# Optimization experiments

Hardware: AMD Instinct MI355X
Metric: run time of the kernel (lower is better)

## Reference

```python
import jax, jax.numpy as jnp
import numpy as np

# Model dims
C = 16          # in_channels / d_model
D_INNER = 64    # expand * C, expand = 64 // C = 4
HEADDIM = 4
NHEADS = D_INNER // HEADDIM   # 16
D_STATE = 64
D_CONV = 4
CONV_DIM = D_INNER + 2 * D_STATE        # 192 (x, B, C streams)
D_IN_PROJ = 2 * D_INNER + 2 * D_STATE + NHEADS  # 272 (z, xBC, dt)
# Input volume
BSZ, DD, HH, WW = 8, 32, 16, 16
L = DD * HH * WW  # 8192, multiple of 256 -> exact adaptive max pool
POOL = 256


def setup_inputs():
    key = jax.random.key(0)
    ks = jax.random.split(key, 10)
    x = jax.random.normal(ks[0], (BSZ, C, DD, HH, WW), jnp.float32)
    # 3 independent Mamba2 blocks -> stack params with leading dim 3
    Win = jax.random.normal(ks[1], (3, D_IN_PROJ, C), jnp.float32) / np.sqrt(C).astype(np.float32)
    conv_w = jax.random.normal(ks[2], (3, CONV_DIM, D_CONV), jnp.float32) / np.sqrt(D_CONV).astype(np.float32)
    conv_b = jax.random.normal(ks[3], (3, CONV_DIM), jnp.float32) * 0.1
    dt_bias = jax.random.normal(ks[4], (3, NHEADS), jnp.float32) * 0.5
    A_log = jnp.log(jax.random.uniform(ks[5], (3, NHEADS), jnp.float32, minval=1.0, maxval=16.0))
    Dp = jax.random.normal(ks[6], (3, NHEADS), jnp.float32) * 0.5 + 1.0
    norm_w = jnp.ones((3, D_INNER), jnp.float32)
    Wout = jax.random.normal(ks[7], (3, C, D_INNER), jnp.float32) / np.sqrt(D_INNER).astype(np.float32)
    gamma = jnp.ones((3, C), jnp.float32)
    beta = jnp.zeros((3, C), jnp.float32)
    lin_w = jax.random.normal(ks[8], (3, 1, C), jnp.float32) / np.sqrt(C).astype(np.float32)
    lin_b = jnp.zeros((3, 1), jnp.float32)
    return dict(x=x, Win=Win, conv_w=conv_w, conv_b=conv_b, dt_bias=dt_bias,
                A_log=A_log, Dp=Dp, norm_w=norm_w, Wout=Wout,
                gamma=gamma, beta=beta, lin_w=lin_w, lin_b=lin_b)


def _mamba2(u, Win, conv_w, conv_b, dt_bias, A_log, Dp, norm_w, Wout):
    """Mamba2 block: u (B, L, C) -> (B, L, C). ngroups=1, rmsnorm gated."""
    B, Lx, _ = u.shape
    zxbcdt = jnp.einsum('blc,pc->blp', u, Win)  # (B, L, 272)
    z = zxbcdt[..., :D_INNER]
    xBC = zxbcdt[..., D_INNER:D_INNER + CONV_DIM]
    dt = jax.nn.softplus(zxbcdt[..., D_INNER + CONV_DIM:] + dt_bias)  # (B, L, H)
    # causal depthwise conv over time
    conv = jax.lax.conv_general_dilated(
        jnp.transpose(xBC, (0, 2, 1)), conv_w[:, None, :], (1,),
        [(D_CONV - 1, 0)], feature_group_count=CONV_DIM)
    xBC = jax.nn.silu(jnp.transpose(conv, (0, 2, 1)) + conv_b)
    xh = xBC[..., :D_INNER].reshape(B, Lx, NHEADS, HEADDIM)
    Bm = xBC[..., D_INNER:D_INNER + D_STATE]   # (B, L, N)
    Cm = xBC[..., D_INNER + D_STATE:]          # (B, L, N)
    A = -jnp.exp(A_log)                        # (H,)
    dA = jnp.exp(dt * A)                       # (B, L, H)
    dtx = dt[..., None] * xh                   # (B, L, H, P)

    def step(S, inp):
        dA_t, dtx_t, B_t, C_t = inp
        S = S * dA_t[:, :, None, None] + dtx_t[..., None] * B_t[:, None, None, :]
        y_t = jnp.einsum('bhpn,bn->bhp', S, C_t)
        return S, y_t

    S0 = jnp.zeros((B, NHEADS, HEADDIM, D_STATE), u.dtype)
    xs = (jnp.moveaxis(dA, 1, 0), jnp.moveaxis(dtx, 1, 0),
          jnp.moveaxis(Bm, 1, 0), jnp.moveaxis(Cm, 1, 0))
    _, ys = jax.lax.scan(step, S0, xs)                       # (L, B, H, P)
    y = jnp.moveaxis(ys, 0, 1) + Dp[None, None, :, None] * xh
    y = y.reshape(B, Lx, D_INNER) * jax.nn.silu(z)           # gate first
    y = y * jax.lax.rsqrt(jnp.mean(y * y, -1, keepdims=True) + 1e-5) * norm_w
    return jnp.einsum('bld,cd->blc', y, Wout)


def _proj_pool(y, gamma, beta, lw, lb):
    """ReLU -> BatchNorm1d (batch stats) -> Linear(C,1) -> AdaptiveMaxPool1d(256)."""
    B, Lx, _ = y.shape
    v = jax.nn.relu(y.reshape(-1, C))
    mu = jnp.mean(v, 0)
    var = jnp.mean((v - mu) ** 2, 0)
    v = (v - mu) * jax.lax.rsqrt(var + 1e-5) * gamma + beta
    s = (v @ lw.T + lb).reshape(B, Lx)
    return jnp.max(s.reshape(B, POOL, Lx // POOL), -1)  # (B, 256)


def reference(x, Win, conv_w, conv_b, dt_bias, A_log, Dp, norm_w, Wout,
              gamma, beta, lin_w, lin_b):
    B, Cc, Dd, Hh, Ww = x.shape
    Lx = Dd * Hh * Ww
    fD = jnp.transpose(x.reshape(B, Cc, Lx), (0, 2, 1))
    fH = jnp.transpose(jnp.transpose(x, (0, 1, 3, 4, 2)).reshape(B, Cc, Lx), (0, 2, 1))
    fW = jnp.transpose(jnp.transpose(x, (0, 1, 4, 2, 3)).reshape(B, Cc, Lx), (0, 2, 1))
    seqs = jnp.stack([fD, fH, fW], 0)  # (3, B, L, C)
    ys = jax.vmap(_mamba2)(seqs, Win, conv_w, conv_b, dt_bias, A_log, Dp, norm_w, Wout)
    pooled = jax.vmap(_proj_pool)(ys, gamma, beta, lin_w, lin_b)  # (3, B, 256)
    return jnp.concatenate([pooled[0], pooled[1], pooled[2]], -1)[:, None, :]  # (B,1,768)
```

## Files before the change

### kernel.cpp

```cpp
#include <hip/hip_runtime.h>
#include <math.h>

#define CONVD 192
#define NC 128
#define PW 32
#define LOG2E 1.4426950408889634f
#define LN2f  0.69314718055994531f

#define OFF_DST   0u
#define OFF_CHA   4194304u
#define OFF_YS    4210688u
#define OFF_PART  5259264u
#define PD        5292032u

#define XSW(m, t)   ((m) * 64 + (((((t) >> 2) ^ ((m) & 15)) & 15) << 2) + ((t) & 3))
#define XSW4(m, tq) ((m) * 64 + ((((tq) ^ ((m) & 15)) & 15) << 2))

typedef float f32x2 __attribute__((ext_vector_type(2)));

__device__ __forceinline__ f32x2 pk_fma(f32x2 a, f32x2 b, f32x2 c) {
    f32x2 d;
    asm("v_pk_fma_f32 %0, %1, %2, %3" : "=v"(d) : "v"(a), "v"(b), "v"(c));
    return d;
}
__device__ __forceinline__ f32x2 pk_fma_alo(f32x2 a, f32x2 b, f32x2 c) {
    f32x2 d;
    asm("v_pk_fma_f32 %0, %1, %2, %3 op_sel_hi:[0,1,1]" : "=v"(d) : "v"(a), "v"(b), "v"(c));
    return d;
}
__device__ __forceinline__ f32x2 pk_fma_ahi(f32x2 a, f32x2 b, f32x2 c) {
    f32x2 d;
    asm("v_pk_fma_f32 %0, %1, %2, %3 op_sel:[1,0,0]" : "=v"(d) : "v"(a), "v"(b), "v"(c));
    return d;
}
__device__ __forceinline__ f32x2 pk_fma_blo(f32x2 a, f32x2 b, f32x2 c) {
    f32x2 d;
    asm("v_pk_fma_f32 %0, %1, %2, %3 op_sel_hi:[1,0,1]" : "=v"(d) : "v"(a), "v"(b), "v"(c));
    return d;
}
__device__ __forceinline__ f32x2 pk_fma_bhi(f32x2 a, f32x2 b, f32x2 c) {
    f32x2 d;
    asm("v_pk_fma_f32 %0, %1, %2, %3 op_sel:[0,1,0]" : "=v"(d) : "v"(a), "v"(b), "v"(c));
    return d;
}
__device__ __forceinline__ f32x2 lo2(float4 v) { f32x2 r; r.x = v.x; r.y = v.y; return r; }
__device__ __forceinline__ f32x2 hi2(float4 v) { f32x2 r; r.x = v.z; r.y = v.w; return r; }

__device__ __forceinline__ float fast_silu(float x) {
    float e = __builtin_amdgcn_exp2f(-x * LOG2E);
    return x * __builtin_amdgcn_rcpf(1.f + e);
}
__device__ __forceinline__ float fast_softplus(float x) {
    if (x > 20.f) return x;
    float e = __builtin_amdgcn_exp2f(x * LOG2E);
    return LN2f * __builtin_amdgcn_logf(1.f + e);
}

template<int NT>
__device__ __forceinline__ void stage_u(
    const float* __restrict__ x, float* u_s, int b, int l0, int dir, int tid)
{
    for (int i = tid; i < 67 * 16; i += NT) {
        int pos = i >> 4, c = i & 15;
        int l = l0 + pos - 3;
        float v = 0.f;
        if (l >= 0) {
            if (dir == 0) {
                v = x[(b * 16 + c) * 8192 + l];
            } else if (dir == 1) {
                int h = l >> 9, w = (l >> 5) & 15, d = l & 31;
                v = x[(((b * 16 + c) * 32 + d) * 16 + h) * 16 + w];
            } else {
                int w = l >> 9, d = (l >> 4) & 31, h = l & 15;
                v = x[(((b * 16 + c) * 32 + d) * 16 + h) * 16 + w];
            }
        }
        u_s[pos * 17 + c] = v;
    }
}

__device__ __forceinline__ float pk_dot16(const f32x2* u2, const float* wp) {
    float4 w0 = *(const float4*)(wp);
    float4 w1 = *(const float4*)(wp + 4);
    float4 w2 = *(const float4*)(wp + 8);
    float4 w3 = *(const float4*)(wp + 12);
    f32x2 a = {0.f, 0.f};
    a = pk_fma(u2[0], lo2(w0), a);
    a = pk_fma(u2[1], hi2(w0), a);
    a = pk_fma(u2[2], lo2(w1), a);
    a = pk_fma(u2[3], hi2(w1), a);
    a = pk_fma(u2[4], lo2(w2), a);
    a = pk_fma(u2[5], hi2(w2), a);
    a = pk_fma(u2[6], lo2(w3), a);
    a = pk_fma(u2[7], hi2(w3), a);
    return a.x + a.y;
}

__global__ __launch_bounds__(512, 6) void k_delta(
    const float* __restrict__ x, const float* __restrict__ Win,
    const float* __restrict__ convw, const float* __restrict__ convb,
    const float* __restrict__ dtb, const float* __restrict__ A_log,
    float* __restrict__ ws, int dir0, int dslm)
{
    __shared__ float u_s[67 * 17];
    __shared__ float xh_c[4096];
    __shared__ float Bs[4096];
    __shared__ float dts[16 * 65];
    __shared__ float wbuf[16 * 65];
    const int tid = threadIdx.x;
    const int ck = blockIdx.x;
    const int b = blockIdx.y;
    const int dir = dir0 + blockIdx.z;
    float* base = ws + (size_t)(dslm * blockIdx.z) * PD;
    float* Dst = base + OFF_DST;
    float* chA = base + OFF_CHA;
    const int l0 = ck * 64;
    float* halo = wbuf;

    stage_u<512>(x, u_s, b, l0, dir, tid);
    __syncthreads();

    const int lane = tid & 63;
    const int wv = __builtin_amdgcn_readfirstlane(tid >> 6);

    f32x2 u2[8];
    {
        const float* ur = &u_s[(lane + 3) * 17];
        #pragma unroll
        for (int k = 0; k < 8; k++) { u2[k].x = ur[2 * k]; u2[k].y = ur[2 * k + 1]; }
    }
    if (tid < 128) {
        f32x2 uh2[8];
        #pragma unroll
        for (int pos = 0; pos < 3; pos++) {
            const float* uhr = &u_s[pos * 17];
            #pragma unroll
            for (int k = 0; k < 8; k++) { uh2[k].x = uhr[2 * k]; uh2[k].y = uhr[2 * k + 1]; }
            halo[pos * 128 + tid] = pk_dot16(uh2, Win + (size_t)(dir * 272 + 64 + tid) * 16);
        }
    }
    __syncthreads();

    for (int i = 0; i < 18; i++) {
        const int g = wv * 18 + i;
        const int col = (g < 128) ? (64 + g) : (256 + (g - 128));
        float acc = pk_dot16(u2, Win + (size_t)(dir * 272 + col) * 16);
        if (col < 256) {
            const int ch = col - 64;
            float v1 = __shfl_up(acc, 1);
            float v2 = __shfl_up(acc, 2);
            float v3 = __shfl_up(acc, 3);
            float hh0 = halo[ch];
            float hh1 = halo[128 + ch];
            float hh2 = halo[256 + ch];
            float m1 = (lane >= 1) ? v1 : hh2;
            float m2 = (lane >= 2) ? v2 : ((lane == 0) ? hh1 : hh2);
            float m3 = (lane >= 3) ? v3 : ((lane == 0) ? hh0 : ((lane == 1) ? hh1 : hh2));
            const float* cwp = convw + (size_t)(dir * CONVD + ch) * 4;
            float conv = convb[dir * CONVD + ch]
                       + cwp[0] * m3 + cwp[1] * m2 + cwp[2] * m1 + cwp[3] * acc;
            float xv = fast_silu(conv);
            if (ch < 64) xh_c[XSW(ch, lane)] = xv;
            else         Bs[XSW(ch - 64, lane)] = xv;
        } else {
            const int h = col - 256;
            dts[h * 65 + lane] = fast_softplus(acc + dtb[dir * 16 + h]);
        }
    }
    __syncthreads();

    for (int h = wv; h < 16; h += 8) {
        float A2 = -expf(A_log[dir * 16 + h]) * LOG2E;
        float dtv = dts[h * 65 + lane];
        float v = dtv * A2;
        #pragma unroll
        for (int off = 1; off < 64; off <<= 1) {
            float o = __shfl_up(v, off, 64);
            if (lane >= off) v += o;
        }
        float tot = __shfl(v, 63, 64);
        wbuf[h * 65 + lane] = __builtin_amdgcn_exp2f(tot - v) * dtv;
        if (lane == 63) chA[(b * 16 + h) * 128 + ck] = __builtin_amdgcn_exp2f(tot);
    }
    __syncthreads();

    for (int j = tid; j < 4096; j += 512) {
        int hp = j >> 6, t = j & 63;
        xh_c[XSW(hp, t)] *= wbuf[(hp >> 2) * 65 + t];
    }
    __syncthreads();

    if (tid < 256) {
        const int hp4 = tid >> 4, n4 = tid & 15;
        f32x2 a2[4][4] = {};
        for (int tq = 0; tq < 16; tq++) {
            float4 xv[4], bv[4];
            #pragma unroll
            for (int i2 = 0; i2 < 4; i2++) {
                xv[i2] = *(const float4*)&xh_c[XSW4(4 * hp4 + i2, tq)];
                bv[i2] = *(const float4*)&Bs[XSW4(4 * n4 + i2, tq)];
            }
            #pragma unroll
            for (int i2 = 0; i2 < 4; i2++)
                #pragma unroll
                for (int j2 = 0; j2 < 4; j2++) {
                    a2[i2][j2] = pk_fma(lo2(xv[i2]), lo2(bv[j2]), a2[i2][j2]);
                    a2[i2][j2] = pk_fma(hi2(xv[i2]), hi2(bv[j2]), a2[i2][j2]);
                }
        }
        #pragma unroll
        for (int i2 = 0; i2 < 4; i2++) {
            int hp = 4 * hp4 + i2;
            int h = hp >> 2, p = hp & 3;
            *(float4*)(Dst + ((size_t)((b * 16 + h) * 128 + ck)) * 256 + p * 64 + 4 * n4) =
                make_float4(a2[i2][0].x + a2[i2][0].y, a2[i2][1].x + a2[i2][1].y,
                            a2[i2][2].x + a2[i2][2].y, a2[i2][3].x + a2[i2][3].y);
        }
    }
}

__global__ __launch_bounds__(64) void k_chunk_scan(
    float* __restrict__ ws, int dslm)
{
    float* base = ws + (size_t)(dslm * blockIdx.z) * PD;
    float* Dst = base + OFF_DST;
    const float* chA = base + OFF_CHA;
    const int bh = blockIdx.x >> 2;
    const int elem = (blockIdx.x & 3) * 64 + threadIdx.x;
    float S = 0.f;
    for (int k0 = 0; k0 < NC; k0 += 8) {
        float d[8], av[8];
        #pragma unroll
        for (int j = 0; j < 8; j++) {
            d[j] = Dst[((size_t)(bh * 128 + k0 + j)) * 256 + elem];
            av[j] = chA[bh * 128 + k0 + j];
        }
        #pragma unroll
        for (int j = 0; j < 8; j++) {
            Dst[((size_t)(bh * 128 + k0 + j)) * 256 + elem] = S;
            S = av[j] * S + d[j];
        }
    }
}

__global__ __launch_bounds__(512, 4) void k_out_epi(
    const float* __restrict__ x, const float* __restrict__ Win,
    const float* __restrict__ convw, const float* __restrict__ convb,
    const float* __restrict__ dtb, const float* __restrict__ A_log,
    const float* __restrict__ Dp, const float* __restrict__ normw,
    const float* __restrict__ Wout, float* __restrict__ ws, int dir0, int dslm)
{
    __shared__ float SinT[64 * 66];
    __shared__ float xh_c[4096];
    __shared__ float Bz[4096];
    __shared__ float Cy[4352];
    __shared__ float uW[67 * 17];
    __shared__ float dts[16 * 68];
    __shared__ float ct2l[16 * 68];
    __shared__ float Dps[16];
    __shared__ float red[4][34];
    float* base = ws + (size_t)(dslm * blockIdx.z) * PD;
    const float* Dst = base + OFF_DST;
    float* ys        = base + OFF_YS;
    float* partials  = base + OFF_PART;
    const int dir = dir0 + blockIdx.z;
    const int tid = threadIdx.x;
    const int b = blockIdx.y;
    const int ck = blockIdx.x;
    const int l0 = ck * 64;
    const int tg = tid & 255;
    const int t4 = tg >> 4, x4 = tg & 15;
    const int grp = tid >> 8;
    const int lane = tid & 63;
    const int wv = __builtin_amdgcn_readfirstlane(tid >> 6);
    float* halo = ct2l;

    stage_u<512>(x, uW, b, l0, dir, tid);
    for (int j = tid; j < 1024; j += 512) {
        int hp = j >> 4, n4 = (j & 15) << 2;
        int h = hp >> 2, p = hp & 3;
        float4 sv = *(const float4*)(Dst + ((size_t)((b * 16 + h) * 128 + ck)) * 256 + p * 64 + n4);
        SinT[(n4 + 0) * 66 + hp] = sv.x;
        SinT[(n4 + 1) * 66 + hp] = sv.y;
        SinT[(n4 + 2) * 66 + hp] = sv.z;
        SinT[(n4 + 3) * 66 + hp] = sv.w;
    }
    if (tid < 16) Dps[tid] = Dp[dir * 16 + tid];
    __syncthreads();

    f32x2 u2[8];
    {
        const float* ur = &uW[(lane + 3) * 17];
        #pragma unroll
        for (int k = 0; k < 8; k++) { u2[k].x = ur[2 * k]; u2[k].y = ur[2 * k + 1]; }
    }
    if (tid < 192) {
        f32x2 uh2[8];
        #pragma unroll
        for (int pos = 0; pos < 3; pos++) {
            const float* uhr = &uW[pos * 17];
            #pragma unroll
            for (int k = 0; k < 8; k++) { uh2[k].x = uhr[2 * k]; uh2[k].y = uhr[2 * k + 1]; }
            halo[pos * 192 + tid] = pk_dot16(uh2, Win + (size_t)(dir * 272 + 64 + tid) * 16);
        }
    }
    __syncthreads();

    for (int i = 0; i < 26; i++) {
        const int col = 64 + wv * 26 + i;
        float acc = pk_dot16(u2, Win + (size_t)(dir * 272 + col) * 16);
        if (col < 256) {
            const int ch = col - 64;
            float v1 = __shfl_up(acc, 1);
            float v2 = __shfl_up(acc, 2);
            float v3 = __shfl_up(acc, 3);
            float hh0 = halo[ch];
            float hh1 = halo[192 + ch];
            float hh2 = halo[384 + ch];
            float m1 = (lane >= 1) ? v1 : hh2;
            float m2 = (lane >= 2) ? v2 : ((lane == 0) ? hh1 : hh2);
            float m3 = (lane >= 3) ? v3 : ((lane == 0) ? hh0 : ((lane == 1) ? hh1 : hh2));
            const float* cwp = convw + (size_t)(dir * CONVD + ch) * 4;
            float conv = convb[dir * CONVD + ch]
                       + cwp[0] * m3 + cwp[1] * m2 + cwp[2] * m1 + cwp[3] * acc;
            float xv = fast_silu(conv);
            if (ch < 64)       xh_c[XSW(ch, lane)] = xv;
            else if (ch < 128) Bz[XSW(ch - 64, lane)] = xv;
            else               Cy[XSW(ch - 128, lane)] = xv;
        } else {
            const int h = col - 256;
            dts[h * 68 + lane] = fast_softplus(acc + dtb[dir * 16 + h]);
        }
    }
    __syncthreads();

    for (int h = wv; h < 16; h += 8) {
        float A2 = -expf(A_log[dir * 16 + h]) * LOG2E;
        float dtv = dts[h * 68 + lane];
        float v = dtv * A2;
        #pragma unroll
        for (int off = 1; off < 64; off <<= 1) {
            float o = __shfl_up(v, off, 64);
            if (lane >= off) v += o;
        }
        ct2l[h * 68 + lane] = v;
    }
    __syncthreads();

    float G_[4][4], CS_[4][4];
    if (grp == 0) {
        f32x2 G2[4][2] = {};
        for (int n = 0; n < 64; n++) {
            float4 cr4 = *(const float4*)&Cy[XSW4(n, t4)];
            float4 br4 = *(const float4*)&Bz[XSW4(n, x4)];
            f32x2 c01 = lo2(cr4), c23 = hi2(cr4);
            f32x2 b01 = lo2(br4), b23 = hi2(br4);
            G2[0][0] = pk_fma_alo(c01, b01, G2[0][0]); G2[0][1] = pk_fma_alo(c01, b23, G2[0][1]);
            G2[1][0] = pk_fma_ahi(c01, b01, G2[1][0]); G2[1][1] = pk_fma_ahi(c01, b23, G2[1][1]);
            G2[2][0] = pk_fma_alo(c23, b01, G2[2][0]); G2[2][1] = pk_fma_alo(c23, b23, G2[2][1]);
            G2[3][0] = pk_fma_ahi(c23, b01, G2[3][0]); G2[3][1] = pk_fma_ahi(c23, b23, G2[3][1]);
        }
        #pragma unroll
        for (int r = 0; r < 4; r++) {
            G_[r][0] = G2[r][0].x; G_[r][1] = G2[r][0].y;
            G_[r][2] = G2[r][1].x; G_[r][3] = G2[r][1].y;
        }
    } else {
        f32x2 C2[4][2] = {};
        for (int n = 0; n < 64; n++) {
            float4 cr4 = *(const float4*)&Cy[XSW4(n, t4)];
            f32x2 c01 = lo2(cr4), c23 = hi2(cr4);
            f32x2 s01 = *(const f32x2*)&SinT[n * 66 + 4 * x4];
            f32x2 s23 = *(const f32x2*)&SinT[n * 66 + 4 * x4 + 2];
            C2[0][0] = pk_fma_alo(c01, s01, C2[0][0]); C2[0][1] = pk_fma_alo(c01, s23, C2[0][1]);
            C2[1][0] = pk_fma_ahi(c01, s01, C2[1][0]); C2[1][1] = pk_fma_ahi(c01, s23, C2[1][1]);
            C2[2][0] = pk_fma_alo(c23, s01, C2[2][0]); C2[2][1] = pk_fma_alo(c23, s23, C2[2][1]);
            C2[3][0] = pk_fma_ahi(c23, s01, C2[3][0]); C2[3][1] = pk_fma_ahi(c23, s23, C2[3][1]);
        }
        #pragma unroll
        for (int r = 0; r < 4; r++) {
            CS_[r][0] = C2[r][0].x; CS_[r][1] = C2[r][0].y;
            CS_[r][2] = C2[r][1].x; CS_[r][3] = C2[r][1].y;
        }
    }
    __syncthreads();

    if (grp == 0) {
        #pragma unroll
        for (int k = 0; k < 16; k++) Cy[k * 257 + tg] = G_[k >> 2][k & 3];
    } else if (x4 < 8) {
        const int idx = t4 * 8 + x4;
        #pragma unroll
        for (int k = 0; k < 16; k++) SinT[k * 129 + idx] = CS_[k >> 2][k & 3];
    }
    __syncthreads();
    if (grp == 1) {
        #pragma unroll
        for (int k = 0; k < 16; k++) G_[k >> 2][k & 3] = Cy[k * 257 + tg];
    } else if (x4 < 8) {
        const int idx = t4 * 8 + x4;
        #pragma unroll
        for (int k = 0; k < 16; k++) CS_[k >> 2][k & 3] = SinT[k * 129 + idx];
    }

    for (int i = 0; i < 8; i++) {
        const int col = wv * 8 + i;
        float acc = pk_dot16(u2, Win + (size_t)(dir * 272 + col) * 16);
        Bz[XSW(col, lane)] = acc;
    }
    for (int j = tid; j < 1024; j += 512) {
        int c = j >> 6, d = j & 63;
        uW[c * 65 + d] = Wout[dir * 1024 + j] * normw[dir * 64 + d];
    }
    __syncthreads();

    float* yv = Cy;
    const int tbase = 4 * t4;
    #pragma unroll 1
    for (int hh = 0; hh < 8; hh++) {
        const int h = 8 * grp + hh;
        const float* ctp = &ct2l[h * 68];
        const float* dtp = &dts[h * 68];
        float4 ctt4 = *(const float4*)&ctp[tbase];
        const float ctt[4] = {ctt4.x, ctt4.y, ctt4.z, ctt4.w};
        float4 cs4 = *(const float4*)&ctp[4 * x4];
        float4 dt4 = *(const float4*)&dtp[4 * x4];
        float4 xq[4];
        #pragma unroll
        for (int p = 0; p < 4; p++) {
            int m = 4 * h + p;
            xq[p] = *(const float4*)&xh_c[m * 64 + (((x4 ^ (m & 15)) & 15) << 2)];
        }
        f32x2 v2[2][4] = {};
        #pragma unroll
        for (int q = 0; q < 4; q++) {
            const int s = 4 * x4 + q;
            float csq = (q == 0) ? cs4.x : (q == 1) ? cs4.y : (q == 2) ? cs4.z : cs4.w;
            float dtq = (q == 0) ? dt4.x : (q == 1) ? dt4.y : (q == 2) ? dt4.z : dt4.w;
            float w[4];
            #pragma unroll
            for (int r = 0; r < 4; r++) {
                float e = __builtin_amdgcn_exp2f(ctt[r] - csq);
                w[r] = (s <= tbase + r) ? (G_[r][q] * dtq) * e : 0.f;
            }
            f32x2 wp0 = {w[0], w[1]};
            f32x2 wp1 = {w[2], w[3]};
            #pragma unroll
            for (int p = 0; p < 4; p++) {
                f32x2 xpair = (q < 2) ? lo2(xq[p]) : hi2(xq[p]);
                if (q & 1) {
                    v2[0][p] = pk_fma_bhi(wp0, xpair, v2[0][p]);
                    v2[1][p] = pk_fma_bhi(wp1, xpair, v2[1][p]);
                } else {
                    v2[0][p] = pk_fma_blo(wp0, xpair, v2[0][p]);
                    v2[1][p] = pk_fma_blo(wp1, xpair, v2[1][p]);
                }
            }
        }
        if (x4 == h) {
            float ect[4];
            #pragma unroll
            for (int r = 0; r < 4; r++) ect[r] = __builtin_amdgcn_exp2f(ctt[r]);
            #pragma unroll
            for (int p = 0; p < 4; p++) {
                v2[0][p].x += ect[0] * CS_[0][p];
                v2[0][p].y += ect[1] * CS_[1][p];
                v2[1][p].x += ect[2] * CS_[2][p];
                v2[1][p].y += ect[3] * CS_[3][p];
            }
        }
        float v[16];
        #pragma unroll
        for (int p = 0; p < 4; p++) {
            v[p]      = v2[0][p].x;
            v[4 + p]  = v2[0][p].y;
            v[8 + p]  = v2[1][p].x;
            v[12 + p] = v2[1][p].y;
        }
        #pragma unroll
        for (int j = 0; j < 8; j++) {
            float a = (x4 & 8) ? v[j + 8] : v[j];
            float s_ = (x4 & 8) ? v[j] : v[j + 8];
            v[j] = a + __shfl_xor(s_, 8);
        }
        #pragma unroll
        for (int j = 0; j < 4; j++) {
            float a = (x4 & 4) ? v[j + 4] : v[j];
            float s_ = (x4 & 4) ? v[j] : v[j + 4];
            v[j] = a + __shfl_xor(s_, 4);
        }
        #pragma unroll
        for (int j = 0; j < 2; j++) {
            float a = (x4 & 2) ? v[j + 2] : v[j];
            float s_ = (x4 & 2) ? v[j] : v[j + 2];
            v[j] = a + __shfl_xor(s_, 2);
        }
        {
            float a = (x4 & 1) ? v[1] : v[0];
            float s_ = (x4 & 1) ? v[0] : v[1];
            v[0] = a + __shfl_xor(s_, 1);
        }
        const int row = tbase + (x4 >> 2);
        yv[(row * 4 + (x4 & 3)) * 17 + h] = v[0];
    }
    __syncthreads();

    float os[4];
    const int row = tid >> 2;
    const int p = tid & 3;
    if (tid < 256) {
        float gg[16], sumsq = 0.f;
        #pragma unroll
        for (int h = 0; h < 16; h++) {
            float yval = yv[(row * 4 + p) * 17 + h];
            int m = 4 * h + p;
            int ax = m * 64 + ((((row >> 2) ^ (m & 15)) & 15) << 2) + (row & 3);
            float xh = xh_c[ax];
            float zv = Bz[ax];
            float val = (yval + Dps[h] * xh) * fast_silu(zv);
            gg[h] = val;
            sumsq += val * val;
        }
        sumsq += __shfl_xor(sumsq, 1);
        sumsq += __shfl_xor(sumsq, 2);
        float rms = rsqrtf(sumsq * (1.f / 64.f) + 1e-5f);

        float oc[16];
        #pragma unroll
        for (int c = 0; c < 16; c++) {
            float a = 0.f;
            #pragma unroll
            for (int h = 0; h < 16; h++) a += gg[h] * uW[c * 65 + 4 * h + p];
            oc[c] = a;
        }
        #pragma unroll
        for (int c = 0; c < 16; c++) {
            oc[c] += __shfl_xor(oc[c], 1);
            oc[c] += __shfl_xor(oc[c], 2);
        }
        #pragma unroll
        for (int i2 = 0; i2 < 4; i2++) {
            float a0 = (p == 0) ? oc[i2] : oc[4 + i2];
            float a1 = (p == 2) ? oc[8 + i2] : oc[12 + i2];
            os[i2] = (((p & 2) == 0) ? a0 : a1) * rms;
        }
        size_t bl = (size_t)(b * 8192 + l0 + row);
        *(float4*)(ys + bl * 16 + 4 * p) = make_float4(os[0], os[1], os[2], os[3]);

        float bs[4], bq[4];
        #pragma unroll
        for (int i2 = 0; i2 < 4; i2++) {
            float vv = fmaxf(os[i2], 0.f);
            bs[i2] = vv;
            bq[i2] = vv * vv;
        }
        #pragma unroll
        for (int off = 4; off < 64; off <<= 1) {
            #pragma unroll
            for (int i2 = 0; i2 < 4; i2++) {
                bs[i2] += __shfl_xor(bs[i2], off);
                bq[i2] += __shfl_xor(bq[i2], off);
            }
        }
        const int wlane = tid & 63, wvid = tid >> 6;
        if (wlane < 4) {
            #pragma unroll
            for (int i2 = 0; i2 < 4; i2++) {
                red[wvid][4 * wlane + i2] = bs[i2];
                red[wvid][16 + 4 * wlane + i2] = bq[i2];
            }
        }
    }
    __syncthreads();
    if (tid < 32) {
        float a = red[0][tid] + red[1][tid] + red[2][tid] + red[3][tid];
        partials[((size_t)(b * 128 + ck)) * 32 + tid] = a;
    }
}

__global__ __launch_bounds__(256) void k_pool_bn(
    const float* __restrict__ gamma, const float* __restrict__ beta,
    const float* __restrict__ lin_w, const float* __restrict__ lin_b,
    float* __restrict__ ws, float* __restrict__ out, int dir0, int dslm)
{
    float* base = ws + (size_t)(dslm * blockIdx.z) * PD;
    const float* ys = base + OFF_YS;
    const float* partials = base + OFF_PART;
    const int dir = dir0 + blockIdx.z;
    const int tid = threadIdx.x;
    __shared__ float red[8][33];
    __shared__ float cf[18];
    {
        int c = tid & 31, ks = tid >> 5;
        float a = 0.f;
        for (int k = ks * 128; k < ks * 128 + 128; k++) a += partials[k * 32 + c];
        red[ks][c] = a;
    }
    __syncthreads();
    if (tid < 32) {
        float a = 0.f;
        #pragma unroll
        for (int s2 = 1; s2 < 8; s2++) a += red[s2][tid];
        red[0][tid] += a;
    }
    __syncthreads();
    if (tid == 0) {
        float off = lin_b[dir];
        for (int c = 0; c < 16; c++) {
            float mu = red[0][c] * (1.f / 65536.f);
            float var = red[0][16 + c] * (1.f / 65536.f) - mu * mu;
            float inv = rsqrtf(var + 1e-5f);
            float coef = inv * gamma[dir * 16 + c] * lin_w[dir * 16 + c];
            cf[c] = coef;
            off += beta[dir * 16 + c] * lin_w[dir * 16 + c] - mu * coef;
        }
        cf[16] = off;
    }
    __syncthreads();

    const int b = blockIdx.x >> 3;
    const int jg = blockIdx.x & 7;
    const int j = jg * 32 + (tid >> 3);
    const int sub = tid & 7;
    float m = -3.4e38f;
    #pragma unroll
    for (int r = 0; r < 4; r++) {
        int l = j * PW + 8 * r + sub;
        const float* rowp = ys + (size_t)(b * 8192 + l) * 16;
        float sv = cf[16];
        #pragma unroll
        for (int k = 0; k < 4; k++) {
            float4 v4 = *(const float4*)(rowp + 4 * k);
            sv += fmaxf(v4.x, 0.f) * cf[4 * k] + fmaxf(v4.y, 0.f) * cf[4 * k + 1]
                + fmaxf(v4.z, 0.f) * cf[4 * k + 2] + fmaxf(v4.w, 0.f) * cf[4 * k + 3];
        }
        m = fmaxf(m, sv);
    }
    m = fmaxf(m, __shfl_xor(m, 1));
    m = fmaxf(m, __shfl_xor(m, 2));
    m = fmaxf(m, __shfl_xor(m, 4));
    if (sub == 0) out[b * 768 + dir * 256 + j] = m;
}

extern "C" void kernel_launch(void* const* d_in, const int* in_sizes, int n_in,
                              void* d_out, int out_size, void* d_ws, size_t ws_size,
                              hipStream_t stream) {
    const float* x     = (const float*)d_in[0];
    const float* Win   = (const float*)d_in[1];
    const float* convw = (const float*)d_in[2];
    const float* convb = (const float*)d_in[3];
    const float* dtb   = (const float*)d_in[4];
    const float* Alog  = (const float*)d_in[5];
    const float* Dp    = (const float*)d_in[6];
    const float* normw = (const float*)d_in[7];
    const float* Wout  = (const float*)d_in[8];
    const float* gamma = (const float*)d_in[9];
    const float* beta  = (const float*)d_in[10];
    const float* linw  = (const float*)d_in[11];
    const float* linb  = (const float*)d_in[12];
    float* out = (float*)d_out;
    float* ws = (float*)d_ws;

    const bool batched = ws_size >= (size_t)3 * PD * 4;
    const int nz = batched ? 3 : 1;
    const int dslm = batched ? 1 : 0;
    const int nloop = batched ? 1 : 3;

    for (int d0 = 0; d0 < nloop; ++d0) {
        k_delta<<<dim3(128, 8, nz), dim3(512), 0, stream>>>(
            x, Win, convw, convb, dtb, Alog, ws, d0, dslm);
        k_chunk_scan<<<dim3(512, 1, nz), dim3(64), 0, stream>>>(ws, dslm);
        k_out_epi<<<dim3(128, 8, nz), dim3(512), 0, stream>>>(
            x, Win, convw, convb, dtb, Alog, Dp, normw, Wout, ws, d0, dslm);
        k_pool_bn<<<dim3(64, 1, nz), dim3(256), 0, stream>>>(
            gamma, beta, linw, linb, ws, out, d0, dslm);
    }
}
```

Baseline: 356.4 us.

## Move C/B Gram and dt cumsum into k_delta, add separate C·S kernel

k_delta now computes the C stream as well. It stores C, the per-chunk C·B^T Gram, the dt values and the cumulative dA to a per-chunk global tile, with the Gram computed by the otherwise idle upper 256 threads. A new k_cs kernel computes C·S_in after the chunk scan. k_out_epi then reads G, C·S, dt and cumsum from the tile instead of recomputing the B/C projections and GEMMs, and its launch bounds are raised to 6 blocks. This moves work off the critical epilogue kernel, but it adds a kernel launch, a much larger workspace, extra global traffic, and lowers k_delta's occupancy hint.

Result: slower. 434.1 us (+21.8%).

```diff
diff --git a/kernel.cpp b/kernel.cpp
--- a/kernel.cpp
+++ b/kernel.cpp
@@ -11,7 +11,14 @@
 #define OFF_CHA   4194304u
 #define OFF_YS    4210688u
 #define OFF_PART  5259264u
-#define PD        5292032u
+#define OFF_TILE  5267456u
+#define PD        19947520u
+
+#define TG  0
+#define TC  4096
+#define TCS 8192
+#define TDT 12288
+#define TCT 13312
 
 #define XSW(m, t)   ((m) * 64 + (((((t) >> 2) ^ ((m) & 15)) & 15) << 2) + ((t) & 3))
 #define XSW4(m, tq) ((m) * 64 + ((((tq) ^ ((m) & 15)) & 15) << 2))
@@ -56,7 +63,7 @@
     return LN2f * __builtin_amdgcn_logf(1.f + e);
 }
 
-template<int NT>
+template<int NT, int STRIDE>
 __device__ __forceinline__ void stage_u(
     const float* __restrict__ x, float* u_s, int b, int l0, int dir, int tid)
 {
@@ -75,7 +82,7 @@
                 v = x[(((b * 16 + c) * 32 + d) * 16 + h) * 16 + w];
             }
         }
-        u_s[pos * 17 + c] = v;
+        u_s[pos * STRIDE + c] = v;
     }
 }
 
@@ -96,7 +103,7 @@
     return a.x + a.y;
 }
 
-__global__ __launch_bounds__(512, 6) void k_delta(
+__global__ __launch_bounds__(512, 4) void k_delta(
     const float* __restrict__ x, const float* __restrict__ Win,
     const float* __restrict__ convw, const float* __restrict__ convb,
     const float* __restrict__ dtb, const float* __restrict__ A_log,
@@ -105,6 +112,7 @@
     __shared__ float u_s[67 * 17];
     __shared__ float xh_c[4096];
     __shared__ float Bs[4096];
+    __shared__ float Cc[4096];
     __shared__ float dts[16 * 65];
     __shared__ float wbuf[16 * 65];
     const int tid = threadIdx.x;
@@ -114,10 +122,11 @@
     float* base = ws + (size_t)(dslm * blockIdx.z) * PD;
     float* Dst = base + OFF_DST;
     float* chA = base + OFF_CHA;
+    float* tile = base + OFF_TILE + (size_t)(b * 128 + ck) * 14336;
     const int l0 = ck * 64;
     float* halo = wbuf;
 
-    stage_u<512>(x, u_s, b, l0, dir, tid);
+    stage_u<512, 17>(x, u_s, b, l0, dir, tid);
     __syncthreads();
 
     const int lane = tid & 63;
@@ -129,185 +138,21 @@
         #pragma unroll
         for (int k = 0; k < 8; k++) { u2[k].x = ur[2 * k]; u2[k].y = ur[2 * k + 1]; }
     }
-    if (tid < 128) {
+    if (tid < 192) {
         f32x2 uh2[8];
         #pragma unroll
         for (int pos = 0; pos < 3; pos++) {
             const float* uhr = &u_s[pos * 17];
             #pragma unroll
             for (int k = 0; k < 8; k++) { uh2[k].x = uhr[2 * k]; uh2[k].y = uhr[2 * k + 1]; }
-            halo[pos * 128 + tid] = pk_dot16(uh2, Win + (size_t)(dir * 272 + 64 + tid) * 16);
-        }
-    }
-    __syncthreads();
-
-    for (int i = 0; i < 18; i++) {
-        const int g = wv * 18 + i;
-        const int col = (g < 128) ? (64 + g) : (256 + (g - 128));
-        float acc = pk_dot16(u2, Win + (size_t)(dir * 272 + col) * 16);
-        if (col < 256) {
-            const int ch = col - 64;
-            float v1 = __shfl_up(acc, 1);
-            float v2 = __shfl_up(acc, 2);
-            float v3 = __shfl_up(acc, 3);
-            float hh0 = halo[ch];
-            float hh1 = halo[128 + ch];
-            float hh2 = halo[256 + ch];
-            float m1 = (lane >= 1) ? v1 : hh2;
-            float m2 = (lane >= 2) ? v2 : ((lane == 0) ? hh1 : hh2);
-            float m3 = (lane >= 3) ? v3 : ((lane == 0) ? hh0 : ((lane == 1) ? hh1 : hh2));
-            const float* cwp = convw + (size_t)(dir * CONVD + ch) * 4;
-            float conv = convb[dir * CONVD + ch]
-                       + cwp[0] * m3 + cwp[1] * m2 + cwp[2] * m1 + cwp[3] * acc;
-            float xv = fast_silu(conv);
-            if (ch < 64) xh_c[XSW(ch, lane)] = xv;
-            else         Bs[XSW(ch - 64, lane)] = xv;
-        } else {
-            const int h = col - 256;
-            dts[h * 65 + lane] = fast_softplus(acc + dtb[dir * 16 + h]);
-        }
-    }
-    __syncthreads();
-
-    for (int h = wv; h < 16; h += 8) {
-        float A2 = -expf(A_log[dir * 16 + h]) * LOG2E;
-        float dtv = dts[h * 65 + lane];
-        float v = dtv * A2;
-        #pragma unroll
-        for (int off = 1; off < 64; off <<= 1) {
-            float o = __shfl_up(v, off, 64);
-            if (lane >= off) v += o;
-        }
-        float tot = __shfl(v, 63, 64);
-        wbuf[h * 65 + lane] = __builtin_amdgcn_exp2f(tot - v) * dtv;
-        if (lane == 63) chA[(b * 16 + h) * 128 + ck] = __builtin_amdgcn_exp2f(tot);
-    }
-    __syncthreads();
-
-    for (int j = tid; j < 4096; j += 512) {
-        int hp = j >> 6, t = j & 63;
-        xh_c[XSW(hp, t)] *= wbuf[(hp >> 2) * 65 + t];
-    }
-    __syncthreads();
-
-    if (tid < 256) {
-        const int hp4 = tid >> 4, n4 = tid & 15;
-        f32x2 a2[4][4] = {};
-        for (int tq = 0; tq < 16; tq++) {
-            float4 xv[4], bv[4];
-            #pragma unroll
-            for (int i2 = 0; i2 < 4; i2++) {
-                xv[i2] = *(const float4*)&xh_c[XSW4(4 * hp4 + i2, tq)];
-                bv[i2] = *(const float4*)&Bs[XSW4(4 * n4 + i2, tq)];
-            }
-            #pragma unroll
-            for (int i2 = 0; i2 < 4; i2++)
-                #pragma unroll
-                for (int j2 = 0; j2 < 4; j2++) {
-                    a2[i2][j2] = pk_fma(lo2(xv[i2]), lo2(bv[j2]), a2[i2][j2]);
-                    a2[i2][j2] = pk_fma(hi2(xv[i2]), hi2(bv[j2]), a2[i2][j2]);
-                }
-        }
-        #pragma unroll
-        for (int i2 = 0; i2 < 4; i2++) {
-            int hp = 4 * hp4 + i2;
-            int h = hp >> 2, p = hp & 3;
-            *(float4*)(Dst + ((size_t)((b * 16 + h) * 128 + ck)) * 256 + p * 64 + 4 * n4) =
-                make_float4(a2[i2][0].x + a2[i2][0].y, a2[i2][1].x + a2[i2][1].y,
-                            a2[i2][2].x + a2[i2][2].y, a2[i2][3].x + a2[i2][3].y);
-        }
-    }
-}
-
-__global__ __launch_bounds__(64) void k_chunk_scan(
-    float* __restrict__ ws, int dslm)
-{
-    float* base = ws + (size_t)(dslm * blockIdx.z) * PD;
-    float* Dst = base + OFF_DST;
-    const float* chA = base + OFF_CHA;
-    const int bh = blockIdx.x >> 2;
-    const int elem = (blockIdx.x & 3) * 64 + threadIdx.x;
-    float S = 0.f;
-    for (int k0 = 0; k0 < NC; k0 += 8) {
-        float d[8], av[8];
-        #pragma unroll
-        for (int j = 0; j < 8; j++) {
-            d[j] = Dst[((size_t)(bh * 128 + k0 + j)) * 256 + elem];
-            av[j] = chA[bh * 128 + k0 + j];
-        }
-        #pragma unroll
-        for (int j = 0; j < 8; j++) {
-            Dst[((size_t)(bh * 128 + k0 + j)) * 256 + elem] = S;
-            S = av[j] * S + d[j];
-        }
-    }
-}
-
-__global__ __launch_bounds__(512, 4) void k_out_epi(
-    const float* __restrict__ x, const float* __restrict__ Win,
-    const float* __restrict__ convw, const float* __restrict__ convb,
-    const float* __restrict__ dtb, const float* __restrict__ A_log,
-    const float* __restrict__ Dp, const float* __restrict__ normw,
-    const float* __restrict__ Wout, float* __restrict__ ws, int dir0, int dslm)
-{
-    __shared__ float SinT[64 * 66];
-    __shared__ float xh_c[4096];
-    __shared__ float Bz[4096];
-    __shared__ float Cy[4352];
-    __shared__ float uW[67 * 17];
-    __shared__ float dts[16 * 68];
-    __shared__ float ct2l[16 * 68];
-    __shared__ float Dps[16];
-    __shared__ float red[4][34];
-    float* base = ws + (size_t)(dslm * blockIdx.z) * PD;
-    const float* Dst = base + OFF_DST;
-    float* ys        = base + OFF_YS;
-    float* partials  = base + OFF_PART;
-    const int dir = dir0 + blockIdx.z;
-    const int tid = threadIdx.x;
-    const int b = blockIdx.y;
-    const int ck = blockIdx.x;
-    const int l0 = ck * 64;
-    const int tg = tid & 255;
-    const int t4 = tg >> 4, x4 = tg & 15;
-    const int grp = tid >> 8;
-    const int lane = tid & 63;
-    const int wv = __builtin_amdgcn_readfirstlane(tid >> 6);
-    float* halo = ct2l;
-
-    stage_u<512>(x, uW, b, l0, dir, tid);
-    for (int j = tid; j < 1024; j += 512) {
-        int hp = j >> 4, n4 = (j & 15) << 2;
-        int h = hp >> 2, p = hp & 3;
-        float4 sv = *(const float4*)(Dst + ((size_t)((b * 16 + h) * 128 + ck)) * 256 + p * 64 + n4);
-        SinT[(n4 + 0) * 66 + hp] = sv.x;
-        SinT[(n4 + 1) * 66 + hp] = sv.y;
-        SinT[(n4 + 2) * 66 + hp] = sv.z;
-        SinT[(n4 + 3) * 66 + hp] = sv.w;
-    }
-    if (tid < 16) Dps[tid] = Dp[dir * 16 + tid];
-    __syncthreads();
-
-    f32x2 u2[8];
-    {
-        const float* ur = &uW[(lane + 3) * 17];
-        #pragma unroll
-        for (int k = 0; k < 8; k++) { u2[k].x = ur[2 * k]; u2[k].y = ur[2 * k + 1]; }
-    }
-    if (tid < 192) {
-        f32x2 uh2[8];
-        #pragma unroll
-        for (int pos = 0; pos < 3; pos++) {
-            const float* uhr = &uW[pos * 17];
-            #pragma unroll
-            for (int k = 0; k < 8; k++) { uh2[k].x = uhr[2 * k]; uh2[k].y = uhr[2 * k + 1]; }
             halo[pos * 192 + tid] = pk_dot16(uh2, Win + (size_t)(dir * 272 + 64 + tid) * 16);
         }
     }
     __syncthreads();
 
     for (int i = 0; i < 26; i++) {
-        const int col = 64 + wv * 26 + i;
+        const int g = wv * 26 + i;
+        const int col = (g < 192) ? (64 + g) : (256 + (g - 192));
         float acc = pk_dot16(u2, Win + (size_t)(dir * 272 + col) * 16);
         if (col < 256) {
             const int ch = col - 64;
@@ -325,34 +170,74 @@
                        + cwp[0] * m3 + cwp[1] * m2 + cwp[2] * m1 + cwp[3] * acc;
             float xv = fast_silu(conv);
             if (ch < 64)       xh_c[XSW(ch, lane)] = xv;
-            else if (ch < 128) Bz[XSW(ch - 64, lane)] = xv;
-            else               Cy[XSW(ch - 128, lane)] = xv;
+            else if (ch < 128) Bs[XSW(ch - 64, lane)] = xv;
+            else               Cc[XSW(ch - 128, lane)] = xv;
         } else {
             const int h = col - 256;
-            dts[h * 68 + lane] = fast_softplus(acc + dtb[dir * 16 + h]);
-        }
-    }
-    __syncthreads();
-
+            float dv = fast_softplus(acc + dtb[dir * 16 + h]);
+            dts[h * 65 + lane] = dv;
+            tile[TDT + h * 64 + lane] = dv;
+        }
+    }
+    __syncthreads();
+
+    for (int j4 = tid; j4 < 1024; j4 += 512)
+        ((float4*)(tile + TC))[j4] = ((const float4*)Cc)[j4];
     for (int h = wv; h < 16; h += 8) {
         float A2 = -expf(A_log[dir * 16 + h]) * LOG2E;
-        float dtv = dts[h * 68 + lane];
+        float dtv = dts[h * 65 + lane];
         float v = dtv * A2;
         #pragma unroll
         for (int off = 1; off < 64; off <<= 1) {
             float o = __shfl_up(v, off, 64);
             if (lane >= off) v += o;
         }
-        ct2l[h * 68 + lane] = v;
-    }
-    __syncthreads();
-
-    float G_[4][4], CS_[4][4];
-    if (grp == 0) {
+        float tot = __shfl(v, 63, 64);
+        tile[TCT + h * 64 + lane] = v;
+        wbuf[h * 65 + lane] = __builtin_amdgcn_exp2f(tot - v) * dtv;
+        if (lane == 63) chA[(b * 16 + h) * 128 + ck] = __builtin_amdgcn_exp2f(tot);
+    }
+    __syncthreads();
+
+    for (int j = tid; j < 4096; j += 512) {
+        int hp = j >> 6, t = j & 63;
+        xh_c[XSW(hp, t)] *= wbuf[(hp >> 2) * 65 + t];
+    }
+    __syncthreads();
+
+    if (tid < 256) {
+        const int hp4 = tid >> 4, n4 = tid & 15;
+        f32x2 a2[4][4] = {};
+        for (int tq = 0; tq < 16; tq++) {
+            float4 xv[4], bv[4];
+            #pragma unroll
+            for (int i2 = 0; i2 < 4; i2++) {
+                xv[i2] = *(const float4*)&xh_c[XSW4(4 * hp4 + i2, tq)];
+                bv[i2] = *(const float4*)&Bs[XSW4(4 * n4 + i2, tq)];
+            }
+            #pragma unroll
+            for (int i2 = 0; i2 < 4; i2++)
+                #pragma unroll
+                for (int j2 = 0; j2 < 4; j2++) {
+                    a2[i2][j2] = pk_fma(lo2(xv[i2]), lo2(bv[j2]), a2[i2][j2]);
+                    a2[i2][j2] = pk_fma(hi2(xv[i2]), hi2(bv[j2]), a2[i2][j2]);
+                }
+        }
+        #pragma unroll
+        for (int i2 = 0; i2 < 4; i2++) {
+            int hp = 4 * hp4 + i2;
+            int h = hp >> 2, p = hp & 3;
+            *(float4*)(Dst + ((size_t)((b * 16 + h) * 128 + ck)) * 256 + p * 64 + 4 * n4) =
+                make_float4(a2[i2][0].x + a2[i2][0].y, a2[i2][1].x + a2[i2][1].y,
+                            a2[i2][2].x + a2[i2][2].y, a2[i2][3].x + a2[i2][3].y);
+        }
+    } else {
+        const int tg2 = tid - 256;
+        const int t4g = tg2 >> 4, x4g = tg2 & 15;
         f32x2 G2[4][2] = {};
         for (int n = 0; n < 64; n++) {
-            float4 cr4 = *(const float4*)&Cy[XSW4(n, t4)];
-            float4 br4 = *(const float4*)&Bz[XSW4(n, x4)];
+            float4 cr4 = *(const float4*)&Cc[XSW4(n, t4g)];
+            float4 br4 = *(const float4*)&Bs[XSW4(n, x4g)];
             f32x2 c01 = lo2(cr4), c23 = hi2(cr4);
             f32x2 b01 = lo2(br4), b23 = hi2(br4);
             G2[0][0] = pk_fma_alo(c01, b01, G2[0][0]); G2[0][1] = pk_fma_alo(c01, b23, G2[0][1]);
@@ -360,53 +245,152 @@
             G2[2][0] = pk_fma_alo(c23, b01, G2[2][0]); G2[2][1] = pk_fma_alo(c23, b23, G2[2][1]);
             G2[3][0] = pk_fma_ahi(c23, b01, G2[3][0]); G2[3][1] = pk_fma_ahi(c23, b23, G2[3][1]);
         }
-        #pragma unroll
-        for (int r = 0; r < 4; r++) {
-            G_[r][0] = G2[r][0].x; G_[r][1] = G2[r][0].y;
-            G_[r][2] = G2[r][1].x; G_[r][3] = G2[r][1].y;
-        }
-    } else {
-        f32x2 C2[4][2] = {};
-        for (int n = 0; n < 64; n++) {
-            float4 cr4 = *(const float4*)&Cy[XSW4(n, t4)];
-            f32x2 c01 = lo2(cr4), c23 = hi2(cr4);
-            f32x2 s01 = *(const f32x2*)&SinT[n * 66 + 4 * x4];
-            f32x2 s23 = *(const f32x2*)&SinT[n * 66 + 4 * x4 + 2];
-            C2[0][0] = pk_fma_alo(c01, s01, C2[0][0]); C2[0][1] = pk_fma_alo(c01, s23, C2[0][1]);
-            C2[1][0] = pk_fma_ahi(c01, s01, C2[1][0]); C2[1][1] = pk_fma_ahi(c01, s23, C2[1][1]);
-            C2[2][0] = pk_fma_alo(c23, s01, C2[2][0]); C2[2][1] = pk_fma_alo(c23, s23, C2[2][1]);
-            C2[3][0] = pk_fma_ahi(c23, s01, C2[3][0]); C2[3][1] = pk_fma_ahi(c23, s23, C2[3][1]);
-        }
-        #pragma unroll
-        for (int r = 0; r < 4; r++) {
-            CS_[r][0] = C2[r][0].x; CS_[r][1] = C2[r][0].y;
-            CS_[r][2] = C2[r][1].x; CS_[r][3] = C2[r][1].y;
-        }
-    }
-    __syncthreads();
-
-    if (grp == 0) {
-        #pragma unroll
-        for (int k = 0; k < 16; k++) Cy[k * 257 + tg] = G_[k >> 2][k & 3];
-    } else if (x4 < 8) {
-        const int idx = t4 * 8 + x4;
-        #pragma unroll
-        for (int k = 0; k < 16; k++) SinT[k * 129 + idx] = CS_[k >> 2][k & 3];
-    }
-    __syncthreads();
-    if (grp == 1) {
-        #pragma unroll
-        for (int k = 0; k < 16; k++) G_[k >> 2][k & 3] = Cy[k * 257 + tg];
-    } else if (x4 < 8) {
-        const int idx = t4 * 8 + x4;
-        #pragma unroll
-        for (int k = 0; k < 16; k++) CS_[k >> 2][k & 3] = SinT[k * 129 + idx];
-    }
+        float* gdst = tile + TG + (size_t)tg2 * 16;
+        #pragma unroll
+        for (int r = 0; r < 4; r++)
+            *(float4*)(gdst + 4 * r) =
+                make_float4(G2[r][0].x, G2[r][0].y, G2[r][1].x, G2[r][1].y);
+    }
+}
+
+__global__ __launch_bounds__(64) void k_chunk_scan(
+    float* __restrict__ ws, int dslm)
+{
+    float* base = ws + (size_t)(dslm * blockIdx.z) * PD;
+    float* Dst = base + OFF_DST;
+    const float* chA = base + OFF_CHA;
+    const int bh = blockIdx.x >> 2;
+    const int elem = (blockIdx.x & 3) * 64 + threadIdx.x;
+    float S = 0.f;
+    for (int k0 = 0; k0 < NC; k0 += 8) {
+        float d[8], av[8];
+        #pragma unroll
+        for (int j = 0; j < 8; j++) {
+            d[j] = Dst[((size_t)(bh * 128 + k0 + j)) * 256 + elem];
+            av[j] = chA[bh * 128 + k0 + j];
+        }
+        #pragma unroll
+        for (int j = 0; j < 8; j++) {
+            Dst[((size_t)(bh * 128 + k0 + j)) * 256 + elem] = S;
+            S = av[j] * S + d[j];
+        }
+    }
+}
+
+__global__ __launch_bounds__(256, 4) void k_cs(
+    float* __restrict__ ws, int dslm)
+{
+    __shared__ float Ci[4096];
+    __shared__ float SinT[64 * 66];
+    float* base = ws + (size_t)(dslm * blockIdx.z) * PD;
+    const float* Dst = base + OFF_DST;
+    float* tile = base + OFF_TILE + (size_t)(blockIdx.y * 128 + blockIdx.x) * 14336;
+    const int tid = threadIdx.x;
+    const int b = blockIdx.y;
+    const int ck = blockIdx.x;
+    const int t4 = tid >> 4, x4 = tid & 15;
+
+    for (int j4 = tid; j4 < 1024; j4 += 256)
+        ((float4*)Ci)[j4] = ((const float4*)(tile + TC))[j4];
+    for (int j = tid; j < 1024; j += 256) {
+        int hp = j >> 4, n4 = (j & 15) << 2;
+        int h = hp >> 2, p = hp & 3;
+        float4 sv = *(const float4*)(Dst + ((size_t)((b * 16 + h) * 128 + ck)) * 256 + p * 64 + n4);
+        SinT[(n4 + 0) * 66 + hp] = sv.x;
+        SinT[(n4 + 1) * 66 + hp] = sv.y;
+        SinT[(n4 + 2) * 66 + hp] = sv.z;
+        SinT[(n4 + 3) * 66 + hp] = sv.w;
+    }
+    __syncthreads();
+
+    f32x2 C2[4][2] = {};
+    for (int n = 0; n < 64; n++) {
+        float4 cr4 = *(const float4*)&Ci[XSW4(n, t4)];
+        f32x2 c01 = lo2(cr4), c23 = hi2(cr4);
+        f32x2 s01 = *(const f32x2*)&SinT[n * 66 + 4 * x4];
+        f32x2 s23 = *(const f32x2*)&SinT[n * 66 + 4 * x4 + 2];
+        C2[0][0] = pk_fma_alo(c01, s01, C2[0][0]); C2[0][1] = pk_fma_alo(c01, s23, C2[0][1]);
+        C2[1][0] = pk_fma_ahi(c01, s01, C2[1][0]); C2[1][1] = pk_fma_ahi(c01, s23, C2[1][1]);
+        C2[2][0] = pk_fma_alo(c23, s01, C2[2][0]); C2[2][1] = pk_fma_alo(c23, s23, C2[2][1]);
+        C2[3][0] = pk_fma_ahi(c23, s01, C2[3][0]); C2[3][1] = pk_fma_ahi(c23, s23, C2[3][1]);
+    }
+    float* cdst = tile + TCS + (size_t)tid * 16;
+    #pragma unroll
+    for (int r = 0; r < 4; r++)
+        *(float4*)(cdst + 4 * r) =
+            make_float4(C2[r][0].x, C2[r][0].y, C2[r][1].x, C2[r][1].y);
+}
+
+__global__ __launch_bounds__(512, 6) void k_out_epi(
+    const float* __restrict__ x, const float* __restrict__ Win,
+    const float* __restrict__ convw, const float* __restrict__ convb,
+    const float* __restrict__ Dp, const float* __restrict__ normw,
+    const float* __restrict__ Wout, float* __restrict__ ws, int dir0, int dslm)
+{
+    __shared__ float uW[67 * 16];
+    __shared__ float xh_c[4096];
+    __shared__ float zc[4096];
+    __shared__ float yv[4096];
+    __shared__ float Dps[16];
+    __shared__ float red[4][34];
+    float* base = ws + (size_t)(dslm * blockIdx.z) * PD;
+    float* ys       = base + OFF_YS;
+    float* partials = base + OFF_PART;
+    const float* tile = base + OFF_TILE + (size_t)(blockIdx.y * 128 + blockIdx.x) * 14336;
+    const int dir = dir0 + blockIdx.z;
+    const int tid = threadIdx.x;
+    const int b = blockIdx.y;
+    const int ck = blockIdx.x;
+    const int l0 = ck * 64;
+    const int tg = tid & 255;
+    const int t4 = tg >> 4, x4 = tg & 15;
+    const int grp = tid >> 8;
+    const int lane = tid & 63;
+    const int wv = __builtin_amdgcn_readfirstlane(tid >> 6);
+    float* halo = yv;
+
+    stage_u<512, 16>(x, uW, b, l0, dir, tid);
+    if (tid < 16) Dps[tid] = Dp[dir * 16 + tid];
+    __syncthreads();
+
+    f32x2 u2[8];
+    {
+        const float* ur = &uW[(lane + 3) * 16];
+        #pragma unroll
+        for (int k = 0; k < 8; k++) { u2[k].x = ur[2 * k]; u2[k].y = ur[2 * k + 1]; }
+    }
+    if (tid < 64) {
+        f32x2 uh2[8];
+        #pragma unroll
+        for (int pos = 0; pos < 3; pos++) {
+            const float* uhr = &uW[pos * 16];
+            #pragma unroll
+            for (int k = 0; k < 8; k++) { uh2[k].x = uhr[2 * k]; uh2[k].y = uhr[2 * k + 1]; }
+            halo[pos * 64 + tid] = pk_dot16(uh2, Win + (size_t)(dir * 272 + 64 + tid) * 16);
+        }
+    }
+    __syncthreads();
 
     for (int i = 0; i < 8; i++) {
         const int col = wv * 8 + i;
-        float acc = pk_dot16(u2, Win + (size_t)(dir * 272 + col) * 16);
-        Bz[XSW(col, lane)] = acc;
+        zc[XSW(col, lane)] = pk_dot16(u2, Win + (size_t)(dir * 272 + col) * 16);
+    }
+    for (int i = 0; i < 8; i++) {
+        const int ch = wv * 8 + i;
+        float acc = pk_dot16(u2, Win + (size_t)(dir * 272 + 64 + ch) * 16);
+        float v1 = __shfl_up(acc, 1);
+        float v2 = __shfl_up(acc, 2);
+        float v3 = __shfl_up(acc, 3);
+        float hh0 = halo[ch];
+        float hh1 = halo[64 + ch];
+        float hh2 = halo[128 + ch];
+        float m1 = (lane >= 1) ? v1 : hh2;
+        float m2 = (lane >= 2) ? v2 : ((lane == 0) ? hh1 : hh2);
+        float m3 = (lane >= 3) ? v3 : ((lane == 0) ? hh0 : ((lane == 1) ? hh1 : hh2));
+        const float* cwp = convw + (size_t)(dir * CONVD + ch) * 4;
+        float conv = convb[dir * CONVD + ch]
+                   + cwp[0] * m3 + cwp[1] * m2 + cwp[2] * m1 + cwp[3] * acc;
+        xh_c[XSW(ch, lane)] = fast_silu(conv);
     }
     for (int j = tid; j < 1024; j += 512) {
         int c = j >> 6, d = j & 63;
@@ -414,17 +398,26 @@
     }
     __syncthreads();
 
-    float* yv = Cy;
+    float G_[4][4];
+    {
+        const float* gsrc = tile + TG + (size_t)tg * 16;
+        #pragma unroll
+        for (int r = 0; r < 4; r++) {
+            float4 g4 = *(const float4*)(gsrc + 4 * r);
+            G_[r][0] = g4.x; G_[r][1] = g4.y; G_[r][2] = g4.z; G_[r][3] = g4.w;
+        }
+    }
+
     const int tbase = 4 * t4;
     #pragma unroll 1
     for (int hh = 0; hh < 8; hh++) {
         const int h = 8 * grp + hh;
-        const float* ctp = &ct2l[h * 68];
-        const float* dtp = &dts[h * 68];
-        float4 ctt4 = *(const float4*)&ctp[tbase];
+        const float* ctp = tile + TCT + h * 64;
+        const float* dtp = tile + TDT + h * 64;
+        float4 ctt4 = *(const float4*)(ctp + tbase);
         const float ctt[4] = {ctt4.x, ctt4.y, ctt4.z, ctt4.w};
-        float4 cs4 = *(const float4*)&ctp[4 * x4];
-        float4 dt4 = *(const float4*)&dtp[4 * x4];
+        float4 cs4 = *(const float4*)(ctp + 4 * x4);
+        float4 dt4 = *(const float4*)(dtp + 4 * x4);
         float4 xq[4];
         #pragma unroll
         for (int p = 0; p < 4; p++) {
@@ -458,15 +451,24 @@
             }
         }
         if (x4 == h) {
+            const float* csrc = tile + TCS + (size_t)tg * 16;
+            float4 c0 = *(const float4*)(csrc);
+            float4 c1 = *(const float4*)(csrc + 4);
+            float4 c2 = *(const float4*)(csrc + 8);
+            float4 c3 = *(const float4*)(csrc + 12);
             float ect[4];
             #pragma unroll
             for (int r = 0; r < 4; r++) ect[r] = __builtin_amdgcn_exp2f(ctt[r]);
+            float cs0[4] = {c0.x, c0.y, c0.z, c0.w};
+            float cs1[4] = {c1.x, c1.y, c1.z, c1.w};
+            float cs2[4] = {c2.x, c2.y, c2.z, c2.w};
+            float cs3[4] = {c3.x, c3.y, c3.z, c3.w};
             #pragma unroll
             for (int p = 0; p < 4; p++) {
-                v2[0][p].x += ect[0] * CS_[0][p];
-                v2[0][p].y += ect[1] * CS_[1][p];
-                v2[1][p].x += ect[2] * CS_[2][p];
-                v2[1][p].y += ect[3] * CS_[3][p];
+                v2[0][p].x += ect[0] * cs0[p];
+                v2[0][p].y += ect[1] * cs1[p];
+                v2[1][p].x += ect[2] * cs2[p];
+                v2[1][p].y += ect[3] * cs3[p];
             }
         }
         float v[16];
@@ -500,8 +502,7 @@
             float s_ = (x4 & 1) ? v[0] : v[1];
             v[0] = a + __shfl_xor(s_, 1);
         }
-        const int row = tbase + (x4 >> 2);
-        yv[(row * 4 + (x4 & 3)) * 17 + h] = v[0];
+        yv[tg * 16 + h] = v[0];
     }
     __syncthreads();
 
@@ -509,15 +510,20 @@
     const int row = tid >> 2;
     const int p = tid & 3;
     if (tid < 256) {
+        float4 ya = *(const float4*)&yv[tid * 16];
+        float4 yb = *(const float4*)&yv[tid * 16 + 4];
+        float4 yc = *(const float4*)&yv[tid * 16 + 8];
+        float4 yd = *(const float4*)&yv[tid * 16 + 12];
+        float yval[16] = {ya.x, ya.y, ya.z, ya.w, yb.x, yb.y, yb.z, yb.w,
+                          yc.x, yc.y, yc.z, yc.w, yd.x, yd.y, yd.z, yd.w};
         float gg[16], sumsq = 0.f;
         #pragma unroll
         for (int h = 0; h < 16; h++) {
-            float yval = yv[(row * 4 + p) * 17 + h];
             int m = 4 * h + p;
             int ax = m * 64 + ((((row >> 2) ^ (m & 15)) & 15) << 2) + (row & 3);
             float xh = xh_c[ax];
-            float zv = Bz[ax];
-            float val = (yval + Dps[h] * xh) * fast_silu(zv);
+            float zv = zc[ax];
+            float val = (yval[h] + Dps[h] * xh) * fast_silu(zv);
             gg[h] = val;
             sumsq += val * val;
         }
@@ -670,8 +676,9 @@
         k_delta<<<dim3(128, 8, nz), dim3(512), 0, stream>>>(
             x, Win, convw, convb, dtb, Alog, ws, d0, dslm);
         k_chunk_scan<<<dim3(512, 1, nz), dim3(64), 0, stream>>>(ws, dslm);
+        k_cs<<<dim3(128, 8, nz), dim3(256), 0, stream>>>(ws, dslm);
         k_out_epi<<<dim3(128, 8, nz), dim3(512), 0, stream>>>(
-            x, Win, convw, convb, dtb, Alog, Dp, normw, Wout, ws, d0, dslm);
+            x, Win, convw, convb, Dp, normw, Wout, ws, d0, dslm);
         k_pool_bn<<<dim3(64, 1, nz), dim3(256), 0, stream>>>(
             gamma, beta, linw, linb, ws, out, d0, dslm);
     }
```
